# Kernel optimization log

Hardware: AMD Instinct MI355X
Metric: run time of the kernel (lower is better)

Reference implementation:

```python
import jax, jax.numpy as jnp
import numpy as np

TEMP = 0.01            # entropy temperature
THRESH = 0.92          # hamming similarity threshold
BETA = 0.25            # commitment weight
ENT_W = 0.1            # entropy loss weight


def _l2_normalize(x, axis=-1, eps=1e-12):
    n = jnp.sqrt(jnp.sum(x * x, axis=axis, keepdims=True))
    return x / jnp.maximum(n, eps)


def _entropy_loss(affinity):
    # affinity: [N, K] codebook affinities (cosine similarities)
    fa = affinity / TEMP
    probs = jax.nn.softmax(fa, axis=-1)
    log_probs = jax.nn.log_softmax(fa + 1e-5, axis=-1)
    avg_probs = jnp.mean(probs, axis=0)
    avg_entropy = -jnp.sum(avg_probs * jnp.log(avg_probs + 1e-5))
    sample_entropy = -jnp.mean(jnp.sum(probs * log_probs, axis=-1))
    return sample_entropy - avg_entropy


def _hamming_consistency_loss(input_blocks, z_e):
    # binary occupancy: non-air voxels -> 1
    binary = (jnp.argmax(input_blocks, axis=1) != 0).astype(jnp.float32)  # [B,24,24,24]
    B = binary.shape[0]
    # faithful to torch: plain reshapes (no transpose)
    patterns = binary.reshape(B, 6, 4, 6, 4, 6, 4).reshape(B, 6, 6, 6, 64).reshape(-1, 64)
    N = patterns.shape[0]
    P = patterns
    # pairwise hamming distance via two Gram matmuls
    ham = P @ (1.0 - P).T + (1.0 - P) @ P.T          # [N,N]
    sim = 1.0 - ham / 64.0
    mask = (sim > THRESH) & (~jnp.eye(N, dtype=bool))
    W = jax.lax.stop_gradient(jnp.where(mask, sim, 0.0))  # detached weights
    # pre-quant embeddings per chunk, l2-normalized; cosine distance matrix
    emb = jnp.transpose(z_e, (0, 2, 3, 4, 1)).reshape(N, -1)  # [N, C]
    en = _l2_normalize(emb, axis=1)
    cos = en @ en.T                                   # [N,N]
    dist = 1.0 - cos
    return jnp.sum(dist * W) / (jnp.sum(W) + 1e-8)


def setup_inputs() -> dict:
    key = jax.random.key(0)
    k1, k2, k3 = jax.random.split(key, 3)
    input_blocks = jax.random.normal(k1, (16, 32, 24, 24, 24), dtype=jnp.float32)
    z_e = jax.random.normal(k2, (16, 256, 6, 6, 6), dtype=jnp.float32)
    codebook = jax.random.normal(k3, (1024, 256), dtype=jnp.float32)
    return {"input_blocks": input_blocks, "z_e": z_e, "codebook": codebook}


def reference(input_blocks, z_e, codebook):
    B, C, H, W, D = z_e.shape
    z = jnp.transpose(z_e, (0, 2, 3, 4, 1)).reshape(-1, C)   # [N, C]
    zn = _l2_normalize(z, axis=1)
    en = _l2_normalize(codebook, axis=1)                      # [K, C]
    affinity = zn @ en.T                                      # [N, K]
    idx = jnp.argmax(affinity, axis=1)                        # max cosine == min L2 on sphere
    z_q = en[idx]                                             # [N, C]
    sg = jax.lax.stop_gradient
    codebook_loss = jnp.mean((z_q - sg(zn)) ** 2)
    commit_loss = BETA * jnp.mean((sg(z_q) - zn) ** 2)
    ent_loss = ENT_W * _entropy_loss(affinity)
    ham_loss = _hamming_consistency_loss(input_blocks, z_e)
    loss = codebook_loss + commit_loss + ent_loss + ham_loss
    # straight-through estimator
    z_q_ste = zn + sg(z_q - zn)
    z_q_out = jnp.transpose(z_q_ste.reshape(B, H, W, D, C), (0, 4, 1, 2, 3))
    return z_q_out, loss, idx
```

## Files before the change

kernel.cpp:

```cpp
#include <hip/hip_runtime.h>
#include <cstdint>
#include <cstddef>

#define N_ROWS 3456
#define C_DIM 256
#define K_CB 1024
#define B_SZ 16
#define SPATIAL 216
#define VOX 13824
#define NCH 32
#define N_GBLK 108
#define N_FBLK 486

typedef __attribute__((ext_vector_type(16))) float f32x16;
typedef __attribute__((ext_vector_type(8))) short bf16x8;

__device__ __forceinline__ unsigned short f2bf_rne(float f) {
    unsigned int u = __float_as_uint(f);
    u += 0x7FFFu + ((u >> 16) & 1u);
    return (unsigned short)(u >> 16);
}
__device__ __forceinline__ float bf2f(unsigned short h) {
    unsigned int u = ((unsigned int)h) << 16;
    return __uint_as_float(u);
}

__device__ __forceinline__ size_t swz(int n, int c) {
    return (size_t)(n >> 5) * 8192 + (size_t)((c >> 3) * 256) + (size_t)((n & 31) * 8) + (c & 7);
}

__global__ __launch_bounds__(256) void k_pre(
        const float* __restrict__ in, const float* __restrict__ cb,
        const float* __restrict__ ze,
        unsigned long long* __restrict__ pats,
        float* __restrict__ scal,
        float* __restrict__ en,
        unsigned short* __restrict__ ehi, unsigned short* __restrict__ elo,
        unsigned short* __restrict__ zhi, unsigned short* __restrict__ zlo) {
    int bid = blockIdx.x;
    int t = threadIdx.x;
    if (bid < 864) {
        if (bid == 0 && t < 16) scal[t] = 0.0f;
        int v = bid * 256 + t;
        int b = v / VOX;
        int r = v % VOX;
        const float* p = in + (size_t)b * NCH * VOX + r;
        float v0 = p[0];
        float mx = -INFINITY;
#pragma unroll
        for (int c = 1; c < NCH; ++c) mx = fmaxf(mx, p[(size_t)c * VOX]);
        unsigned long long m = __ballot(mx > v0);
        if ((t & 63) == 0) pats[v >> 6] = m;
        return;
    }
    __shared__ float ws[16];
    if (bid < 1888) {
        int k = bid - 864, c = t;
        float v = cb[k * C_DIM + c];
        float ss = v * v;
#pragma unroll
        for (int off = 32; off > 0; off >>= 1) ss += __shfl_down(ss, off, 64);
        if ((c & 63) == 0) ws[c >> 6] = ss;
        __syncthreads();
        float nrm = fmaxf(sqrtf(ws[0] + ws[1] + ws[2] + ws[3]), 1e-12f);
        float o = v / nrm;
        en[k * C_DIM + c] = o;
        unsigned short h = f2bf_rne(o);
        size_t off = swz(k, c);
        ehi[off] = h;
        elo[off] = f2bf_rne(o - bf2f(h));
    } else {
        int zb = bid - 1888;
        int n0 = zb * 4;
        int b = n0 / SPATIAL, s0 = n0 - b * SPATIAL;
        int c = t, w = t >> 6, lane = t & 63;
        float4 v4 = *(const float4*)&ze[((size_t)(b * C_DIM + c)) * SPATIAL + s0];
        float q0 = v4.x * v4.x, q1 = v4.y * v4.y, q2 = v4.z * v4.z, q3 = v4.w * v4.w;
#pragma unroll
        for (int off = 32; off > 0; off >>= 1) {
            q0 += __shfl_down(q0, off, 64);
            q1 += __shfl_down(q1, off, 64);
            q2 += __shfl_down(q2, off, 64);
            q3 += __shfl_down(q3, off, 64);
        }
        if (lane == 0) {
            ws[w * 4 + 0] = q0; ws[w * 4 + 1] = q1;
            ws[w * 4 + 2] = q2; ws[w * 4 + 3] = q3;
        }
        __syncthreads();
        float vv[4] = {v4.x, v4.y, v4.z, v4.w};
#pragma unroll
        for (int j = 0; j < 4; ++j) {
            float nrm = fmaxf(sqrtf(ws[j] + ws[4 + j] + ws[8 + j] + ws[12 + j]), 1e-12f);
            float o = vv[j] / nrm;
            unsigned short h = f2bf_rne(o);
            size_t off = swz(n0 + j, c);
            zhi[off] = h;
            zlo[off] = f2bf_rne(o - bf2f(h));
        }
    }
}

__global__ __launch_bounds__(512) void k_fat(
        const unsigned short* __restrict__ zhi, const unsigned short* __restrict__ zlo,
        const unsigned short* __restrict__ ehi, const unsigned short* __restrict__ elo,
        const unsigned long long* __restrict__ pats,
        const float* __restrict__ en,
        float* __restrict__ avgp_part, float* __restrict__ scal,
        float* __restrict__ out) {
    __shared__ float zq[32 * 257];
    __shared__ float sm[32][8];
    __shared__ int   si[32][8];
    __shared__ float sS[32][8];
    __shared__ float sT[32][8];
    __shared__ float gm[32];
    __shared__ int   gmi[32];
    __shared__ float invS[32];
    __shared__ float ws8[8];
    __shared__ float hw8[8], hd8[8];
    __shared__ int lastflag;
    unsigned int* done = (unsigned int*)&scal[8];

    int t = threadIdx.x;
    int w = t >> 6, lane = t & 63;
    int half = lane >> 5, l31 = lane & 31;
    int bid = blockIdx.x;
    const bf16x8* __restrict__ Zh = (const bf16x8*)zhi;
    const bf16x8* __restrict__ Zl = (const bf16x8*)zlo;
    const bf16x8* __restrict__ Eh = (const bf16x8*)ehi;
    const bf16x8* __restrict__ El = (const bf16x8*)elo;

    if (bid < N_GBLK) {
        int sa = bid;
        int n0 = bid * 32;

        f32x16 acc[4];
#pragma unroll
        for (int q = 0; q < 4; ++q)
#pragma unroll
            for (int e = 0; e < 16; ++e) acc[q][e] = 0.0f;

#pragma unroll
        for (int s16 = 0; s16 < 16; ++s16) {
            int u = s16 * 64 + lane;
            bf16x8 ah = Zh[(size_t)sa * 1024 + u];
            bf16x8 al = Zl[(size_t)sa * 1024 + u];
            bf16x8 bh[4], bl[4];
#pragma unroll
            for (int q = 0; q < 4; ++q) {
                bh[q] = Eh[(size_t)(w * 4 + q) * 1024 + u];
                bl[q] = El[(size_t)(w * 4 + q) * 1024 + u];
            }
#pragma unroll
            for (int q = 0; q < 4; ++q) {
                acc[q] = __builtin_amdgcn_mfma_f32_32x32x16_bf16(ah, bh[q], acc[q], 0, 0, 0);
                acc[q] = __builtin_amdgcn_mfma_f32_32x32x16_bf16(ah, bl[q], acc[q], 0, 0, 0);
                acc[q] = __builtin_amdgcn_mfma_f32_32x32x16_bf16(al, bh[q], acc[q], 0, 0, 0);
            }
        }

#pragma unroll
        for (int g = 0; g < 16; ++g) {
            float m = acc[0][g];
            int mi = w * 128 + l31;
#pragma unroll
            for (int q = 1; q < 4; ++q) {
                float x = acc[q][g];
                int c = w * 128 + q * 32 + l31;
                if (x > m) { m = x; mi = c; }
            }
#pragma unroll
            for (int mask = 1; mask < 32; mask <<= 1) {
                float vo = __shfl_xor(m, mask, 64);
                int   io = __shfl_xor(mi, mask, 64);
                if (vo > m || (vo == m && io < mi)) { m = vo; mi = io; }
            }
            int row = (g & 3) + 8 * (g >> 2) + 4 * half;
            if (l31 == 0) { sm[row][w] = m; si[row][w] = mi; }
        }
        __syncthreads();

        float cmv = 0.0f;
        if (t < 32) {
            float m = sm[t][0];
            int mi = si[t][0];
#pragma unroll
            for (int ww = 1; ww < 8; ++ww) {
                float mw = sm[t][ww];
                int miw = si[t][ww];
                if (mw > m || (mw == m && miw < mi)) { m = mw; mi = miw; }
            }
            gm[t] = m; gmi[t] = mi;
            out[884737 + n0 + t] = (float)mi;
            cmv = 2.0f - 2.0f * m;
        }
        if (w == 0) {
#pragma unroll
            for (int off = 32; off > 0; off >>= 1) cmv += __shfl_down(cmv, off, 64);
            if (lane == 0) atomicAdd(&scal[1], cmv);
        }
        __syncthreads();

#pragma unroll
        for (int g = 0; g < 16; ++g) {
            int row = (g & 3) + 8 * (g >> 2) + 4 * half;
            float gmr = gm[row];
            float S = 0.0f, T = 0.0f;
#pragma unroll
            for (int q = 0; q < 4; ++q) {
                float d = 100.0f * (acc[q][g] - gmr);
                float ee = __expf(d);
                S += ee; T += ee * d;
                acc[q][g] = ee;
            }
#pragma unroll
            for (int mask = 1; mask < 32; mask <<= 1) {
                S += __shfl_xor(S, mask, 64);
                T += __shfl_xor(T, mask, 64);
            }
            if (l31 == 0) { sS[row][w] = S; sT[row][w] = T; }
        }
#pragma unroll
        for (int rr = 0; rr < 4; ++rr) {
            int row = w * 4 + rr;
            int mi = gmi[row];
            float4 g4 = *(const float4*)&en[(size_t)mi * C_DIM + lane * 4];
            zq[row * 257 + lane * 4 + 0] = g4.x;
            zq[row * 257 + lane * 4 + 1] = g4.y;
            zq[row * 257 + lane * 4 + 2] = g4.z;
            zq[row * 257 + lane * 4 + 3] = g4.w;
        }
        __syncthreads();

        float sev = 0.0f;
        if (t < 32) {
            float S = 0.0f, T = 0.0f;
#pragma unroll
            for (int ww = 0; ww < 8; ++ww) { S += sS[t][ww]; T += sT[t][ww]; }
            float iv = 1.0f / S;
            invS[t] = iv;
            sev = logf(S) - T * iv;
        }
        if (w == 0) {
#pragma unroll
            for (int off = 32; off > 0; off >>= 1) sev += __shfl_down(sev, off, 64);
            if (lane == 0) atomicAdd(&scal[0], sev);
        }
        __syncthreads();

        {
            float cs[4] = {0.0f, 0.0f, 0.0f, 0.0f};
#pragma unroll
            for (int g = 0; g < 16; ++g) {
                int row = (g & 3) + 8 * (g >> 2) + 4 * half;
                float iv = invS[row];
#pragma unroll
                for (int q = 0; q < 4; ++q) cs[q] += acc[q][g] * iv;
            }
#pragma unroll
            for (int q = 0; q < 4; ++q) cs[q] += __shfl_xor(cs[q], 32, 64);
            if (half == 0) {
#pragma unroll
                for (int q = 0; q < 4; ++q)
                    avgp_part[(size_t)bid * K_CB + w * 128 + q * 32 + l31] = cs[q];
            }
        }

        {
            int rl = t & 31, cg = t >> 5;
            int n = n0 + rl;
            int b = n / SPATIAL, s = n - b * SPATIAL;
            size_t obase = ((size_t)b * C_DIM) * SPATIAL + s;
#pragma unroll
            for (int cc = 0; cc < 16; ++cc) {
                int c = cg * 16 + cc;
                out[obase + (size_t)c * SPATIAL] = zq[rl * 257 + c];
            }
        }
    } else {
        int hb = bid - N_GBLK;
        int ti = 0, rem = hb;
        while (rem >= 27 - ti) { rem -= 27 - ti; ++ti; }
        int tj = ti + rem;
        int i0 = ti * 128, j0 = tj * 128;
        float factor = (ti == tj) ? 1.0f : 2.0f;
        int iw = w & 3, kh = w >> 2;
        int sib = ti * 4 + iw;
        int sjb = tj * 4;

        f32x16 acc[4];
#pragma unroll
        for (int c = 0; c < 4; ++c)
#pragma unroll
            for (int e = 0; e < 16; ++e) acc[c][e] = 0.0f;

#pragma unroll
        for (int s8 = 0; s8 < 8; ++s8) {
            int u = (kh * 8 + s8) * 64 + lane;
            bf16x8 a0 = Zh[(size_t)sib * 1024 + u];
            bf16x8 bf[4];
#pragma unroll
            for (int c = 0; c < 4; ++c)
                bf[c] = Zh[(size_t)(sjb + c) * 1024 + u];
#pragma unroll
            for (int c = 0; c < 4; ++c)
                acc[c] = __builtin_amdgcn_mfma_f32_32x32x16_bf16(a0, bf[c], acc[c], 0, 0, 0);
        }

        unsigned long long pj[4];
#pragma unroll
        for (int c = 0; c < 4; ++c) pj[c] = pats[j0 + c * 32 + l31];

        float sW = 0.0f, sD = 0.0f;
        int ibase = i0 + iw * 32 + 4 * half;
#pragma unroll
        for (int g = 0; g < 16; ++g) {
            int gi = ibase + (g & 3) + 8 * (g >> 2);
            unsigned long long pi = pats[gi];
#pragma unroll
            for (int c = 0; c < 4; ++c) {
                int gj = j0 + c * 32 + l31;
                int pop = __popcll(pi ^ pj[c]);
                float wgt = (pop <= 5 && gi != gj) ? (1.0f - (float)pop * 0.015625f) : 0.0f;
                sW += wgt;
                sD += wgt * acc[c][g];
            }
        }
#pragma unroll
        for (int off = 32; off > 0; off >>= 1) {
            sW += __shfl_down(sW, off, 64);
            sD += __shfl_down(sD, off, 64);
        }
        if (lane == 0) { hw8[w] = sW; hd8[w] = sD; }
        __syncthreads();
        if (t == 0) {
            float W = hw8[0] + hw8[1] + hw8[2] + hw8[3];
            float D = hd8[0] + hd8[1] + hd8[2] + hd8[3]
                    + hd8[4] + hd8[5] + hd8[6] + hd8[7];
            atomicAdd(&scal[2], factor * W);
            atomicAdd(&scal[3], factor * D);
        }
    }

    __syncthreads();
    if (t == 0) {
        __threadfence();
        unsigned int old = atomicAdd(done, 1u);
        lastflag = (old == N_FBLK - 1) ? 1 : 0;
    }
    __syncthreads();
    if (lastflag) {
        __threadfence();
        int col0 = t, col1 = t + 512;
        float p0 = 0.0f, p1 = 0.0f, p2 = 0.0f, p3 = 0.0f;
        float q0 = 0.0f, q1 = 0.0f, q2 = 0.0f, q3 = 0.0f;
        for (int bb = 0; bb < N_GBLK; bb += 4) {
            p0 += avgp_part[(size_t)(bb + 0) * K_CB + col0];
            p1 += avgp_part[(size_t)(bb + 1) * K_CB + col0];
            p2 += avgp_part[(size_t)(bb + 2) * K_CB + col0];
            p3 += avgp_part[(size_t)(bb + 3) * K_CB + col0];
            q0 += avgp_part[(size_t)(bb + 0) * K_CB + col1];
            q1 += avgp_part[(size_t)(bb + 1) * K_CB + col1];
            q2 += avgp_part[(size_t)(bb + 2) * K_CB + col1];
            q3 += avgp_part[(size_t)(bb + 3) * K_CB + col1];
        }
        float ap0 = (p0 + p1 + p2 + p3) * (1.0f / N_ROWS);
        float ap1 = (q0 + q1 + q2 + q3) * (1.0f / N_ROWS);
        float term = ap0 * logf(ap0 + 1e-5f) + ap1 * logf(ap1 + 1e-5f);
#pragma unroll
        for (int off = 32; off > 0; off >>= 1) term += __shfl_down(term, off, 64);
        if (lane == 0) ws8[w] = term;
        __syncthreads();
        if (t == 0) {
            float sAP = 0.0f;
#pragma unroll
            for (int i = 0; i < 8; ++i) sAP += ws8[i];
            float s0 = atomicAdd(&scal[0], 0.0f);
            float s1 = atomicAdd(&scal[1], 0.0f);
            float s2 = atomicAdd(&scal[2], 0.0f);
            float s3 = atomicAdd(&scal[3], 0.0f);
            float sample = s0 * (1.0f / N_ROWS);
            float commit = s1 * (1.0f / ((float)N_ROWS * C_DIM));
            float ent = 0.1f * (sample + sAP);
            float ham = (s2 - s3) / (s2 + 1e-8f);
            out[884736] = 1.25f * commit + ent + ham;
        }
    }
}

extern "C" void kernel_launch(void* const* d_in, const int* in_sizes, int n_in,
                              void* d_out, int out_size, void* d_ws, size_t ws_size,
                              hipStream_t stream) {
    const float* in_blocks = (const float*)d_in[0];
    const float* z_e       = (const float*)d_in[1];
    const float* cb        = (const float*)d_in[2];
    float* out = (float*)d_out;

    char* ws = (char*)d_ws;
    float* en   = (float*)(ws + 0);
    unsigned short* zhi = (unsigned short*)(ws + 15204352);
    unsigned short* zlo = (unsigned short*)(ws + 16973824);
    unsigned short* ehi = (unsigned short*)(ws + 18743296);
    unsigned short* elo = (unsigned short*)(ws + 19267584);
    unsigned long long* pats = (unsigned long long*)(ws + 19791872);
    float* avgp_part = (float*)(ws + 19819520);
    float* scal = (float*)(ws + 20704256);

    k_pre<<<2752, 256, 0, stream>>>(in_blocks, cb, z_e, pats, scal,
                                    en, ehi, elo, zhi, zlo);
    k_fat<<<N_FBLK, 512, 0, stream>>>(zhi, zlo, ehi, elo, pats, en,
                                      avgp_part, scal, out);
}
```

Measured before the change: 130.5 us.

## Double k_fat block size to 1024 threads, halving per-wave work

Launches the fused kernel with 16 waves per block instead of 8. Each wave now covers 64 codebook columns in the affinity block and a quarter of the K dimension in the Hamming Gram block, with the reductions and shared arrays widened to match. The preprocessing argmax loads all 32 channels into registers before reducing, to expose more memory-level parallelism. The aim is more parallelism and latency hiding per block, at the cost of more cross-wave reduction, larger shared arrays and tighter register limits.

```diff
diff --git a/kernel.cpp b/kernel.cpp
--- a/kernel.cpp
+++ b/kernel.cpp
@@ -45,10 +45,13 @@
         int b = v / VOX;
         int r = v % VOX;
         const float* p = in + (size_t)b * NCH * VOX + r;
-        float v0 = p[0];
-        float mx = -INFINITY;
-#pragma unroll
-        for (int c = 1; c < NCH; ++c) mx = fmaxf(mx, p[(size_t)c * VOX]);
+        float vals[NCH];
+#pragma unroll
+        for (int c = 0; c < NCH; ++c) vals[c] = p[(size_t)c * VOX];
+        float v0 = vals[0];
+        float mx = vals[1];
+#pragma unroll
+        for (int c = 2; c < NCH; ++c) mx = fmaxf(mx, vals[c]);
         unsigned long long m = __ballot(mx > v0);
         if ((t & 63) == 0) pats[v >> 6] = m;
         return;
@@ -101,7 +104,7 @@
     }
 }
 
-__global__ __launch_bounds__(512) void k_fat(
+__global__ __launch_bounds__(1024) void k_fat(
         const unsigned short* __restrict__ zhi, const unsigned short* __restrict__ zlo,
         const unsigned short* __restrict__ ehi, const unsigned short* __restrict__ elo,
         const unsigned long long* __restrict__ pats,
@@ -109,15 +112,15 @@
         float* __restrict__ avgp_part, float* __restrict__ scal,
         float* __restrict__ out) {
     __shared__ float zq[32 * 257];
-    __shared__ float sm[32][8];
-    __shared__ int   si[32][8];
-    __shared__ float sS[32][8];
-    __shared__ float sT[32][8];
+    __shared__ float sm[32][16];
+    __shared__ int   si[32][16];
+    __shared__ float sS[32][16];
+    __shared__ float sT[32][16];
     __shared__ float gm[32];
     __shared__ int   gmi[32];
     __shared__ float invS[32];
-    __shared__ float ws8[8];
-    __shared__ float hw8[8], hd8[8];
+    __shared__ float ws16[16];
+    __shared__ float hw16[16], hd16[16];
     __shared__ int lastflag;
     unsigned int* done = (unsigned int*)&scal[8];
 
@@ -134,9 +137,9 @@
         int sa = bid;
         int n0 = bid * 32;
 
-        f32x16 acc[4];
-#pragma unroll
-        for (int q = 0; q < 4; ++q)
+        f32x16 acc[2];
+#pragma unroll
+        for (int q = 0; q < 2; ++q)
 #pragma unroll
             for (int e = 0; e < 16; ++e) acc[q][e] = 0.0f;
 
@@ -145,14 +148,14 @@
             int u = s16 * 64 + lane;
             bf16x8 ah = Zh[(size_t)sa * 1024 + u];
             bf16x8 al = Zl[(size_t)sa * 1024 + u];
-            bf16x8 bh[4], bl[4];
-#pragma unroll
-            for (int q = 0; q < 4; ++q) {
-                bh[q] = Eh[(size_t)(w * 4 + q) * 1024 + u];
-                bl[q] = El[(size_t)(w * 4 + q) * 1024 + u];
-            }
-#pragma unroll
-            for (int q = 0; q < 4; ++q) {
+            bf16x8 bh[2], bl[2];
+#pragma unroll
+            for (int q = 0; q < 2; ++q) {
+                bh[q] = Eh[(size_t)(w * 2 + q) * 1024 + u];
+                bl[q] = El[(size_t)(w * 2 + q) * 1024 + u];
+            }
+#pragma unroll
+            for (int q = 0; q < 2; ++q) {
                 acc[q] = __builtin_amdgcn_mfma_f32_32x32x16_bf16(ah, bh[q], acc[q], 0, 0, 0);
                 acc[q] = __builtin_amdgcn_mfma_f32_32x32x16_bf16(ah, bl[q], acc[q], 0, 0, 0);
                 acc[q] = __builtin_amdgcn_mfma_f32_32x32x16_bf16(al, bh[q], acc[q], 0, 0, 0);
@@ -162,11 +165,11 @@
 #pragma unroll
         for (int g = 0; g < 16; ++g) {
             float m = acc[0][g];
-            int mi = w * 128 + l31;
-#pragma unroll
-            for (int q = 1; q < 4; ++q) {
+            int mi = w * 64 + l31;
+#pragma unroll
+            for (int q = 1; q < 2; ++q) {
                 float x = acc[q][g];
-                int c = w * 128 + q * 32 + l31;
+                int c = w * 64 + q * 32 + l31;
                 if (x > m) { m = x; mi = c; }
             }
 #pragma unroll
@@ -185,7 +188,7 @@
             float m = sm[t][0];
             int mi = si[t][0];
 #pragma unroll
-            for (int ww = 1; ww < 8; ++ww) {
+            for (int ww = 1; ww < 16; ++ww) {
                 float mw = sm[t][ww];
                 int miw = si[t][ww];
                 if (mw > m || (mw == m && miw < mi)) { m = mw; mi = miw; }
@@ -207,7 +210,7 @@
             float gmr = gm[row];
             float S = 0.0f, T = 0.0f;
 #pragma unroll
-            for (int q = 0; q < 4; ++q) {
+            for (int q = 0; q < 2; ++q) {
                 float d = 100.0f * (acc[q][g] - gmr);
                 float ee = __expf(d);
                 S += ee; T += ee * d;
@@ -221,8 +224,8 @@
             if (l31 == 0) { sS[row][w] = S; sT[row][w] = T; }
         }
 #pragma unroll
-        for (int rr = 0; rr < 4; ++rr) {
-            int row = w * 4 + rr;
+        for (int rr = 0; rr < 2; ++rr) {
+            int row = w * 2 + rr;
             int mi = gmi[row];
             float4 g4 = *(const float4*)&en[(size_t)mi * C_DIM + lane * 4];
             zq[row * 257 + lane * 4 + 0] = g4.x;
@@ -236,7 +239,7 @@
         if (t < 32) {
             float S = 0.0f, T = 0.0f;
 #pragma unroll
-            for (int ww = 0; ww < 8; ++ww) { S += sS[t][ww]; T += sT[t][ww]; }
+            for (int ww = 0; ww < 16; ++ww) { S += sS[t][ww]; T += sT[t][ww]; }
             float iv = 1.0f / S;
             invS[t] = iv;
             sev = logf(S) - T * iv;
@@ -249,20 +252,20 @@
         __syncthreads();
 
         {
-            float cs[4] = {0.0f, 0.0f, 0.0f, 0.0f};
+            float cs[2] = {0.0f, 0.0f};
 #pragma unroll
             for (int g = 0; g < 16; ++g) {
                 int row = (g & 3) + 8 * (g >> 2) + 4 * half;
                 float iv = invS[row];
 #pragma unroll
-                for (int q = 0; q < 4; ++q) cs[q] += acc[q][g] * iv;
-            }
-#pragma unroll
-            for (int q = 0; q < 4; ++q) cs[q] += __shfl_xor(cs[q], 32, 64);
+                for (int q = 0; q < 2; ++q) cs[q] += acc[q][g] * iv;
+            }
+#pragma unroll
+            for (int q = 0; q < 2; ++q) cs[q] += __shfl_xor(cs[q], 32, 64);
             if (half == 0) {
 #pragma unroll
-                for (int q = 0; q < 4; ++q)
-                    avgp_part[(size_t)bid * K_CB + w * 128 + q * 32 + l31] = cs[q];
+                for (int q = 0; q < 2; ++q)
+                    avgp_part[(size_t)bid * K_CB + w * 64 + q * 32 + l31] = cs[q];
             }
         }
 
@@ -272,8 +275,8 @@
             int b = n / SPATIAL, s = n - b * SPATIAL;
             size_t obase = ((size_t)b * C_DIM) * SPATIAL + s;
 #pragma unroll
-            for (int cc = 0; cc < 16; ++cc) {
-                int c = cg * 16 + cc;
+            for (int cc = 0; cc < 8; ++cc) {
+                int c = cg * 8 + cc;
                 out[obase + (size_t)c * SPATIAL] = zq[rl * 257 + c];
             }
         }
@@ -284,7 +287,7 @@
         int tj = ti + rem;
         int i0 = ti * 128, j0 = tj * 128;
         float factor = (ti == tj) ? 1.0f : 2.0f;
-        int iw = w & 3, kh = w >> 2;
+        int iw = w & 3, kq = w >> 2;
         int sib = ti * 4 + iw;
         int sjb = tj * 4;
 
@@ -295,8 +298,8 @@
             for (int e = 0; e < 16; ++e) acc[c][e] = 0.0f;
 
 #pragma unroll
-        for (int s8 = 0; s8 < 8; ++s8) {
-            int u = (kh * 8 + s8) * 64 + lane;
+        for (int s4 = 0; s4 < 4; ++s4) {
+            int u = (kq * 4 + s4) * 64 + lane;
             bf16x8 a0 = Zh[(size_t)sib * 1024 + u];
             bf16x8 bf[4];
 #pragma unroll
@@ -331,12 +334,13 @@
             sW += __shfl_down(sW, off, 64);
             sD += __shfl_down(sD, off, 64);
         }
-        if (lane == 0) { hw8[w] = sW; hd8[w] = sD; }
+        if (lane == 0) { hw16[w] = sW; hd16[w] = sD; }
         __syncthreads();
         if (t == 0) {
-            float W = hw8[0] + hw8[1] + hw8[2] + hw8[3];
-            float D = hd8[0] + hd8[1] + hd8[2] + hd8[3]
-                    + hd8[4] + hd8[5] + hd8[6] + hd8[7];
+            float W = hw16[0] + hw16[1] + hw16[2] + hw16[3];
+            float D = 0.0f;
+#pragma unroll
+            for (int i = 0; i < 16; ++i) D += hd16[i];
             atomicAdd(&scal[2], factor * W);
             atomicAdd(&scal[3], factor * D);
         }
@@ -351,30 +355,24 @@
     __syncthreads();
     if (lastflag) {
         __threadfence();
-        int col0 = t, col1 = t + 512;
+        int col = t;
         float p0 = 0.0f, p1 = 0.0f, p2 = 0.0f, p3 = 0.0f;
-        float q0 = 0.0f, q1 = 0.0f, q2 = 0.0f, q3 = 0.0f;
         for (int bb = 0; bb < N_GBLK; bb += 4) {
-            p0 += avgp_part[(size_t)(bb + 0) * K_CB + col0];
-            p1 += avgp_part[(size_t)(bb + 1) * K_CB + col0];
-            p2 += avgp_part[(size_t)(bb + 2) * K_CB + col0];
-            p3 += avgp_part[(size_t)(bb + 3) * K_CB + col0];
-            q0 += avgp_part[(size_t)(bb + 0) * K_CB + col1];
-            q1 += avgp_part[(size_t)(bb + 1) * K_CB + col1];
-            q2 += avgp_part[(size_t)(bb + 2) * K_CB + col1];
-            q3 += avgp_part[(size_t)(bb + 3) * K_CB + col1];
-        }
-        float ap0 = (p0 + p1 + p2 + p3) * (1.0f / N_ROWS);
-        float ap1 = (q0 + q1 + q2 + q3) * (1.0f / N_ROWS);
-        float term = ap0 * logf(ap0 + 1e-5f) + ap1 * logf(ap1 + 1e-5f);
+            p0 += avgp_part[(size_t)(bb + 0) * K_CB + col];
+            p1 += avgp_part[(size_t)(bb + 1) * K_CB + col];
+            p2 += avgp_part[(size_t)(bb + 2) * K_CB + col];
+            p3 += avgp_part[(size_t)(bb + 3) * K_CB + col];
+        }
+        float ap = (p0 + p1 + p2 + p3) * (1.0f / N_ROWS);
+        float term = ap * logf(ap + 1e-5f);
 #pragma unroll
         for (int off = 32; off > 0; off >>= 1) term += __shfl_down(term, off, 64);
-        if (lane == 0) ws8[w] = term;
+        if (lane == 0) ws16[w] = term;
         __syncthreads();
         if (t == 0) {
             float sAP = 0.0f;
 #pragma unroll
-            for (int i = 0; i < 8; ++i) sAP += ws8[i];
+            for (int i = 0; i < 16; ++i) sAP += ws16[i];
             float s0 = atomicAdd(&scal[0], 0.0f);
             float s1 = atomicAdd(&scal[1], 0.0f);
             float s2 = atomicAdd(&scal[2], 0.0f);
@@ -408,6 +406,6 @@
 
     k_pre<<<2752, 256, 0, stream>>>(in_blocks, cb, z_e, pats, scal,
                                     en, ehi, elo, zhi, zlo);
-    k_fat<<<N_FBLK, 512, 0, stream>>>(zhi, zlo, ehi, elo, pats, en,
-                                      avgp_part, scal, out);
-}
+    k_fat<<<N_FBLK, 1024, 0, stream>>>(zhi, zlo, ehi, elo, pats, en,
+                                       avgp_part, scal, out);
+}
```

Result: slower. 139.2 us (+6.6%).

## Stage codebook tiles via global_load_lds and vectorize occupancy argmax loads

Applied to the files above, without the earlier changes.

The codebook-affinity GEMM blocks in k_fat now stage each K-slice of the bf16 hi/lo codebook and z tiles into shared memory with direct global-to-LDS loads, then read MFMA operands from LDS instead of each wave fetching from global. This trades redundant global loads for two barriers per K-step and a larger 66 KB shared buffer. k_pre's occupancy pass now processes two voxels per thread with float2 loads and packs bits through shared-memory atomicOr, halving its block count. launch_bounds adds a min-blocks hint of 4.

```diff
diff --git a/kernel.cpp b/kernel.cpp
--- a/kernel.cpp
+++ b/kernel.cpp
@@ -23,6 +23,13 @@
 __device__ __forceinline__ float bf2f(unsigned short h) {
     unsigned int u = ((unsigned int)h) << 16;
     return __uint_as_float(u);
+}
+
+__device__ __forceinline__ void gload_lds16(const void* g, void* l) {
+    __builtin_amdgcn_global_load_lds(
+        (const __attribute__((address_space(1))) void*)g,
+        (__attribute__((address_space(3))) void*)l,
+        16, 0, 0);
 }
 
 __device__ __forceinline__ size_t swz(int n, int c) {
@@ -39,23 +46,35 @@
         unsigned short* __restrict__ zhi, unsigned short* __restrict__ zlo) {
     int bid = blockIdx.x;
     int t = threadIdx.x;
-    if (bid < 864) {
+    if (bid < 432) {
         if (bid == 0 && t < 16) scal[t] = 0.0f;
-        int v = bid * 256 + t;
-        int b = v / VOX;
-        int r = v % VOX;
+        __shared__ unsigned long long wpk[8];
+        if (t < 8) wpk[t] = 0ULL;
+        __syncthreads();
+        int v0i = bid * 512 + t * 2;
+        int b = v0i / VOX;
+        int r = v0i % VOX;
         const float* p = in + (size_t)b * NCH * VOX + r;
-        float v0 = p[0];
-        float mx = -INFINITY;
-#pragma unroll
-        for (int c = 1; c < NCH; ++c) mx = fmaxf(mx, p[(size_t)c * VOX]);
-        unsigned long long m = __ballot(mx > v0);
-        if ((t & 63) == 0) pats[v >> 6] = m;
+        float2 vals[NCH];
+#pragma unroll
+        for (int c = 0; c < NCH; ++c)
+            vals[c] = *(const float2*)&p[(size_t)c * VOX];
+        float m0 = vals[1].x, m1 = vals[1].y;
+#pragma unroll
+        for (int c = 2; c < NCH; ++c) {
+            m0 = fmaxf(m0, vals[c].x);
+            m1 = fmaxf(m1, vals[c].y);
+        }
+        unsigned long long bits = (m0 > vals[0].x ? 1ULL : 0ULL)
+                                | (m1 > vals[0].y ? 2ULL : 0ULL);
+        atomicOr(&wpk[t >> 5], bits << ((t & 31) * 2));
+        __syncthreads();
+        if (t < 8) pats[(bid * 512 >> 6) + t] = wpk[t];
         return;
     }
     __shared__ float ws[16];
-    if (bid < 1888) {
-        int k = bid - 864, c = t;
+    if (bid < 1456) {
+        int k = bid - 432, c = t;
         float v = cb[k * C_DIM + c];
         float ss = v * v;
 #pragma unroll
@@ -70,7 +89,7 @@
         ehi[off] = h;
         elo[off] = f2bf_rne(o - bf2f(h));
     } else {
-        int zb = bid - 1888;
+        int zb = bid - 1456;
         int n0 = zb * 4;
         int b = n0 / SPATIAL, s0 = n0 - b * SPATIAL;
         int c = t, w = t >> 6, lane = t & 63;
@@ -101,14 +120,14 @@
     }
 }
 
-__global__ __launch_bounds__(512) void k_fat(
+__global__ __launch_bounds__(512, 4) void k_fat(
         const unsigned short* __restrict__ zhi, const unsigned short* __restrict__ zlo,
         const unsigned short* __restrict__ ehi, const unsigned short* __restrict__ elo,
         const unsigned long long* __restrict__ pats,
         const float* __restrict__ en,
         float* __restrict__ avgp_part, float* __restrict__ scal,
         float* __restrict__ out) {
-    __shared__ float zq[32 * 257];
+    __shared__ __align__(16) char smem[67584];
     __shared__ float sm[32][8];
     __shared__ int   si[32][8];
     __shared__ float sS[32][8];
@@ -120,19 +139,21 @@
     __shared__ float hw8[8], hd8[8];
     __shared__ int lastflag;
     unsigned int* done = (unsigned int*)&scal[8];
+    float* zq = (float*)smem;
 
     int t = threadIdx.x;
     int w = t >> 6, lane = t & 63;
     int half = lane >> 5, l31 = lane & 31;
     int bid = blockIdx.x;
-    const bf16x8* __restrict__ Zh = (const bf16x8*)zhi;
-    const bf16x8* __restrict__ Zl = (const bf16x8*)zlo;
-    const bf16x8* __restrict__ Eh = (const bf16x8*)ehi;
-    const bf16x8* __restrict__ El = (const bf16x8*)elo;
 
     if (bid < N_GBLK) {
         int sa = bid;
         int n0 = bid * 32;
+        const char* EHb = (const char*)ehi;
+        const char* ELb = (const char*)elo;
+        const char* ZHb = (const char*)zhi;
+        const char* ZLb = (const char*)zlo;
+        const bf16x8* SB = (const bf16x8*)smem;
 
         f32x16 acc[4];
 #pragma unroll
@@ -140,16 +161,28 @@
 #pragma unroll
             for (int e = 0; e < 16; ++e) acc[q][e] = 0.0f;
 
-#pragma unroll
+        size_t lanebyte = (size_t)lane * 16;
         for (int s16 = 0; s16 < 16; ++s16) {
-            int u = s16 * 64 + lane;
-            bf16x8 ah = Zh[(size_t)sa * 1024 + u];
-            bf16x8 al = Zl[(size_t)sa * 1024 + u];
+            size_t kb = (size_t)s16 * 1024;
+#pragma unroll
+            for (int j = 0; j < 9; ++j) {
+                int i = w + j * 8;
+                if (i >= 66) break;
+                const char* g;
+                if (i < 32)       g = EHb + (size_t)i * 16384 + kb + lanebyte;
+                else if (i < 64)  g = ELb + (size_t)(i - 32) * 16384 + kb + lanebyte;
+                else if (i == 64) g = ZHb + (size_t)sa * 16384 + kb + lanebyte;
+                else              g = ZLb + (size_t)sa * 16384 + kb + lanebyte;
+                gload_lds16(g, (void*)(smem + i * 1024));
+            }
+            __syncthreads();
+            bf16x8 ah = SB[64 * 64 + lane];
+            bf16x8 al = SB[65 * 64 + lane];
             bf16x8 bh[4], bl[4];
 #pragma unroll
             for (int q = 0; q < 4; ++q) {
-                bh[q] = Eh[(size_t)(w * 4 + q) * 1024 + u];
-                bl[q] = El[(size_t)(w * 4 + q) * 1024 + u];
+                bh[q] = SB[(w * 4 + q) * 64 + lane];
+                bl[q] = SB[(32 + w * 4 + q) * 64 + lane];
             }
 #pragma unroll
             for (int q = 0; q < 4; ++q) {
@@ -157,6 +190,7 @@
                 acc[q] = __builtin_amdgcn_mfma_f32_32x32x16_bf16(ah, bl[q], acc[q], 0, 0, 0);
                 acc[q] = __builtin_amdgcn_mfma_f32_32x32x16_bf16(al, bh[q], acc[q], 0, 0, 0);
             }
+            __syncthreads();
         }
 
 #pragma unroll
@@ -278,6 +312,7 @@
             }
         }
     } else {
+        const bf16x8* Zh = (const bf16x8*)zhi;
         int hb = bid - N_GBLK;
         int ti = 0, rem = hb;
         while (rem >= 27 - ti) { rem -= 27 - ti; ++ti; }
@@ -406,7 +441,7 @@
     float* avgp_part = (float*)(ws + 19819520);
     float* scal = (float*)(ws + 20704256);
 
-    k_pre<<<2752, 256, 0, stream>>>(in_blocks, cb, z_e, pats, scal,
+    k_pre<<<2320, 256, 0, stream>>>(in_blocks, cb, z_e, pats, scal,
                                     en, ehi, elo, zhi, zlo);
     k_fat<<<N_FBLK, 512, 0, stream>>>(zhi, zlo, ehi, elo, pats, en,
                                       avgp_part, scal, out);
```

New measurement: 142.8 us. 1.09x slower.

## Vectorize occupancy argmax, remap fat blocks across XCDs, stagger K-loop start

Applied to the files above, without the earlier changes.

The occupancy pass now handles two voxels per thread with float2 loads across all 32 channels and packs the bits through a shared atomicOr, which halves the block count in the pre-kernel. The fused kernel remaps block IDs so that codebook-GEMM blocks and Hamming blocks are spread evenly over the 8 XCDs. Each block also rotates the starting index of its K-loop so that concurrent blocks do not hit the same L2/HBM lines together. The cost is one extra shared-memory sync and atomics per block, plus higher register use from holding 32 float2 values per thread.

```diff
diff --git a/kernel.cpp b/kernel.cpp
--- a/kernel.cpp
+++ b/kernel.cpp
@@ -39,23 +39,35 @@
         unsigned short* __restrict__ zhi, unsigned short* __restrict__ zlo) {
     int bid = blockIdx.x;
     int t = threadIdx.x;
-    if (bid < 864) {
+    if (bid < 432) {
         if (bid == 0 && t < 16) scal[t] = 0.0f;
-        int v = bid * 256 + t;
-        int b = v / VOX;
-        int r = v % VOX;
+        __shared__ unsigned long long wpk[8];
+        if (t < 8) wpk[t] = 0ULL;
+        __syncthreads();
+        int v0i = bid * 512 + t * 2;
+        int b = v0i / VOX;
+        int r = v0i % VOX;
         const float* p = in + (size_t)b * NCH * VOX + r;
-        float v0 = p[0];
-        float mx = -INFINITY;
-#pragma unroll
-        for (int c = 1; c < NCH; ++c) mx = fmaxf(mx, p[(size_t)c * VOX]);
-        unsigned long long m = __ballot(mx > v0);
-        if ((t & 63) == 0) pats[v >> 6] = m;
+        float2 vals[NCH];
+#pragma unroll
+        for (int c = 0; c < NCH; ++c)
+            vals[c] = *(const float2*)&p[(size_t)c * VOX];
+        float m0 = vals[1].x, m1 = vals[1].y;
+#pragma unroll
+        for (int c = 2; c < NCH; ++c) {
+            m0 = fmaxf(m0, vals[c].x);
+            m1 = fmaxf(m1, vals[c].y);
+        }
+        unsigned long long bits = (m0 > vals[0].x ? 1ULL : 0ULL)
+                                | (m1 > vals[0].y ? 2ULL : 0ULL);
+        atomicOr(&wpk[t >> 5], bits << ((t & 31) * 2));
+        __syncthreads();
+        if (t < 8) pats[(bid * 512 >> 6) + t] = wpk[t];
         return;
     }
     __shared__ float ws[16];
-    if (bid < 1888) {
-        int k = bid - 864, c = t;
+    if (bid < 1456) {
+        int k = bid - 432, c = t;
         float v = cb[k * C_DIM + c];
         float ss = v * v;
 #pragma unroll
@@ -70,7 +82,7 @@
         ehi[off] = h;
         elo[off] = f2bf_rne(o - bf2f(h));
     } else {
-        int zb = bid - 1888;
+        int zb = bid - 1456;
         int n0 = zb * 4;
         int b = n0 / SPATIAL, s0 = n0 - b * SPATIAL;
         int c = t, w = t >> 6, lane = t & 63;
@@ -124,7 +136,17 @@
     int t = threadIdx.x;
     int w = t >> 6, lane = t & 63;
     int half = lane >> 5, l31 = lane & 31;
-    int bid = blockIdx.x;
+
+    int bid0 = blockIdx.x;
+    int xcd = bid0 & 7, slot = bid0 >> 3;
+    int bid;
+    if (bid0 < 432) {
+        if (xcd < 2) bid = slot * 2 + xcd;
+        else         bid = N_GBLK + slot * 6 + (xcd - 2);
+    } else {
+        bid = N_GBLK + 324 + (bid0 - 432);
+    }
+
     const bf16x8* __restrict__ Zh = (const bf16x8*)zhi;
     const bf16x8* __restrict__ Zl = (const bf16x8*)zlo;
     const bf16x8* __restrict__ Eh = (const bf16x8*)ehi;
@@ -133,6 +155,7 @@
     if (bid < N_GBLK) {
         int sa = bid;
         int n0 = bid * 32;
+        int boff = (bid * 5) & 15;
 
         f32x16 acc[4];
 #pragma unroll
@@ -141,7 +164,8 @@
             for (int e = 0; e < 16; ++e) acc[q][e] = 0.0f;
 
 #pragma unroll
-        for (int s16 = 0; s16 < 16; ++s16) {
+        for (int s = 0; s < 16; ++s) {
+            int s16 = (s + boff) & 15;
             int u = s16 * 64 + lane;
             bf16x8 ah = Zh[(size_t)sa * 1024 + u];
             bf16x8 al = Zl[(size_t)sa * 1024 + u];
@@ -287,6 +311,7 @@
         int iw = w & 3, kh = w >> 2;
         int sib = ti * 4 + iw;
         int sjb = tj * 4;
+        int hoff = hb & 7;
 
         f32x16 acc[4];
 #pragma unroll
@@ -296,7 +321,7 @@
 
 #pragma unroll
         for (int s8 = 0; s8 < 8; ++s8) {
-            int u = (kh * 8 + s8) * 64 + lane;
+            int u = (kh * 8 + ((s8 + hoff) & 7)) * 64 + lane;
             bf16x8 a0 = Zh[(size_t)sib * 1024 + u];
             bf16x8 bf[4];
 #pragma unroll
@@ -406,7 +431,7 @@
     float* avgp_part = (float*)(ws + 19819520);
     float* scal = (float*)(ws + 20704256);
 
-    k_pre<<<2752, 256, 0, stream>>>(in_blocks, cb, z_e, pats, scal,
+    k_pre<<<2320, 256, 0, stream>>>(in_blocks, cb, z_e, pats, scal,
                                     en, ehi, elo, zhi, zlo);
     k_fat<<<N_FBLK, 512, 0, stream>>>(zhi, zlo, ehi, elo, pats, en,
                                       avgp_part, scal, out);
```

Result: slower. 153.8 us (+17.8%).
